# Optimization experiments

Hardware: AMD Instinct MI355X
Metric: run time of the kernel (lower is better)

Reference implementation:

```python
import jax, jax.numpy as jnp
import numpy as np

B, S, D, H = 4, 2048, 1024, 16
DH = D // H  # head dim = dim_k = dim_v


def setup_inputs() -> dict:
    key = jax.random.key(0)
    ks = jax.random.split(key, 8)
    return {
        "query": jax.random.normal(ks[0], (B, S, D), jnp.float32),
        "key": jax.random.normal(ks[1], (B, S, D), jnp.float32),
        "value": jax.random.normal(ks[2], (B, S, D), jnp.float32),
        # per-head projection weights, stacked over heads: [H, D, DH]
        "Wq": jax.random.normal(ks[3], (H, D, DH), jnp.float32) / np.sqrt(D),
        "Wk": jax.random.normal(ks[4], (H, D, DH), jnp.float32) / np.sqrt(D),
        "Wv": jax.random.normal(ks[5], (H, D, DH), jnp.float32) / np.sqrt(D),
        "Wo": jax.random.normal(ks[6], (D, D), jnp.float32) / np.sqrt(D),
        "bo": jax.random.normal(ks[7], (D,), jnp.float32) * 0.01,
        "is_causal": 1,
    }


def reference(query, key, value, Wq, Wk, Wv, Wo, bo, is_causal):
    # Per-head projections, batched over heads via einsum.  [B,H,S,DH]
    q = jnp.einsum("bsd,hdk->bhsk", query, Wq)
    k = jnp.einsum("bsd,hdk->bhsk", key, Wk)
    v = jnp.einsum("bsd,hdk->bhsk", value, Wv)
    scores = jnp.einsum("bhqk,bhsk->bhqs", q, k) / jnp.sqrt(jnp.float32(DH))
    if is_causal:
        mask = jnp.triu(jnp.ones((S, S), bool), k=1)  # strict upper tri
        scores = jnp.where(mask, -jnp.inf, scores)
    attn = jax.nn.softmax(scores, axis=-1)
    out = jnp.einsum("bhqs,bhsk->bhqk", attn, v)
    # concat heads along last dim == [B,S,H*DH], then output projection
    out = out.transpose(0, 2, 1, 3).reshape(B, S, D)
    return out @ Wo.T + bo
```

## Files before the change

kernel.cpp:

```cpp
#include <hip/hip_runtime.h>
#include <hip/hip_bf16.h>
#include <stdint.h>

typedef __bf16 bf16_t;
typedef __bf16 bf16x4 __attribute__((ext_vector_type(4)));
typedef __bf16 bf16x8 __attribute__((ext_vector_type(8)));
typedef float  f32x4  __attribute__((ext_vector_type(4)));

#define B_   4
#define S_   2048
#define D_   1024
#define H_   16
#define DH_  64
#define MTOT (B_ * S_)
#define NITEMS 1024
#define NPERS  768

__device__ __forceinline__ void gload_lds16(const void* g, void* l) {
  __builtin_amdgcn_global_load_lds((const __attribute__((address_space(1))) void*)g,
                                   (__attribute__((address_space(3))) void*)l,
                                   16, 0, 0);
}

__global__ __launch_bounds__(256) void k_cvt(const float* __restrict__ in,
                                             bf16_t* __restrict__ out, int n8) {
  for (int i = blockIdx.x * blockDim.x + threadIdx.x; i < n8;
       i += gridDim.x * blockDim.x) {
    const float4* p = (const float4*)(in + (size_t)i * 8);
    float4 a = p[0], b = p[1];
    bf16x8 o;
    o[0] = (bf16_t)a.x; o[1] = (bf16_t)a.y; o[2] = (bf16_t)a.z; o[3] = (bf16_t)a.w;
    o[4] = (bf16_t)b.x; o[5] = (bf16_t)b.y; o[6] = (bf16_t)b.z; o[7] = (bf16_t)b.w;
    *(bf16x8*)(out + (size_t)i * 8) = o;
  }
}

__global__ __launch_bounds__(256) void k_pack(const float* __restrict__ Wq,
                                              const float* __restrict__ Wk,
                                              const float* __restrict__ Wv,
                                              bf16_t* __restrict__ Wt) {
  const int z = blockIdx.z;
  const float* W = (z == 0) ? Wq : ((z == 1) ? Wk : Wv);
  const float scale = (z == 0) ? 0.125f : 1.0f;
  const int h  = blockIdx.y;
  const int d0 = blockIdx.x * 64;

  __shared__ float tile[64][65];
  const int t  = threadIdx.x;
  const int r  = t >> 2;
  const int c0 = (t & 3) * 16;

  const float* src = W + ((size_t)h * D_ + d0 + r) * DH_ + c0;
#pragma unroll
  for (int j4 = 0; j4 < 4; ++j4) {
    float4 v = *(const float4*)(src + j4 * 4);
    tile[r][c0 + j4 * 4 + 0] = v.x;
    tile[r][c0 + j4 * 4 + 1] = v.y;
    tile[r][c0 + j4 * 4 + 2] = v.z;
    tile[r][c0 + j4 * 4 + 3] = v.w;
  }
  __syncthreads();

  const int kk = r, dd0 = c0;
  bf16_t* dst = Wt + ((size_t)z * D_ + h * DH_ + kk) * D_ + d0 + dd0;
  bf16x8 o0, o1;
#pragma unroll
  for (int j = 0; j < 8; ++j) {
    o0[j] = (bf16_t)(tile[dd0 + j][kk] * scale);
    o1[j] = (bf16_t)(tile[dd0 + 8 + j][kk] * scale);
  }
  *(bf16x8*)(dst)     = o0;
  *(bf16x8*)(dst + 8) = o1;
}

template <int MODE>
__global__ __launch_bounds__(256) void k_gemm(
    const bf16_t* __restrict__ A0, const bf16_t* __restrict__ A1,
    const bf16_t* __restrict__ A2, const bf16_t* __restrict__ W,
    bf16_t* __restrict__ O0, bf16_t* __restrict__ O1, bf16_t* __restrict__ O2,
    float* __restrict__ OF, const float* __restrict__ bias,
    int M, int N, int K) {
  const int z = blockIdx.z;
  const bf16_t* A  = (MODE == 0) ? (z == 0 ? A0 : (z == 1 ? A1 : A2)) : A0;
  const bf16_t* Bt = (MODE == 0) ? (W + (size_t)z * N * K) : W;
  bf16_t* OB = (MODE == 0) ? (z == 0 ? O0 : (z == 1 ? O1 : O2)) : nullptr;

  __shared__ bf16_t As[128 * 32];
  __shared__ bf16_t Bs[128 * 32];

  const int tid  = threadIdx.x;
  const int w    = tid >> 6, lane = tid & 63;
  const int wm   = w >> 1,   wn   = w & 1;
  const int g    = lane >> 4, cl  = lane & 15;
  const int m0   = blockIdx.x * 128, n0 = blockIdx.y * 128;
  const int r_a  = lane >> 2;
  const int c_a  = (lane & 3) * 8;

  f32x4 acc[4][4] = {};

  for (int k0 = 0; k0 < K; k0 += 32) {
#pragma unroll
    for (int it = 0; it < 2; ++it) {
      const int c16 = it * 4 + w;
      const int row = c16 * 16 + r_a;
      gload_lds16(A  + (size_t)(m0 + row) * K + (k0 + c_a),
                  (bf16_t*)((char*)As + c16 * 1024));
      gload_lds16(Bt + (size_t)(n0 + row) * K + (k0 + c_a),
                  (bf16_t*)((char*)Bs + c16 * 1024));
    }
    __syncthreads();

    bf16x8 af[4], bfv[4];
#pragma unroll
    for (int mi = 0; mi < 4; ++mi)
      af[mi] = *(const bf16x8*)&As[(wm * 64 + mi * 16 + cl) * 32 + g * 8];
#pragma unroll
    for (int ni = 0; ni < 4; ++ni)
      bfv[ni] = *(const bf16x8*)&Bs[(wn * 64 + ni * 16 + cl) * 32 + g * 8];
#pragma unroll
    for (int mi = 0; mi < 4; ++mi)
#pragma unroll
      for (int ni = 0; ni < 4; ++ni)
        acc[mi][ni] = __builtin_amdgcn_mfma_f32_16x16x32_bf16(
            af[mi], bfv[ni], acc[mi][ni], 0, 0, 0);
    __syncthreads();
  }

#pragma unroll
  for (int mi = 0; mi < 4; ++mi) {
#pragma unroll
    for (int ni = 0; ni < 4; ++ni) {
      const int col = n0 + wn * 64 + ni * 16 + cl;
#pragma unroll
      for (int i = 0; i < 4; ++i) {
        const int row = m0 + wm * 64 + mi * 16 + g * 4 + i;
        if (MODE == 0)
          OB[(size_t)row * N + col] = (bf16_t)acc[mi][ni][i];
        else
          OF[(size_t)row * N + col] = acc[mi][ni][i] + bias[col];
      }
    }
  }
}

__global__ __launch_bounds__(256, 3) void k_attn(const bf16_t* __restrict__ Qp,
                                                 const bf16_t* __restrict__ Kp,
                                                 const bf16_t* __restrict__ Vp,
                                                 bf16_t* __restrict__ AO,
                                                 int* __restrict__ wq_ctr,
                                                 const int* __restrict__ causal_p) {
  __shared__ bf16_t Ks[64 * 72];
  __shared__ bf16_t Vs[2 * 64 * 64];
  __shared__ bf16_t Vt[64 * 72];
  __shared__ bf16_t Pb[4][32 * 72];
  __shared__ int s_item;

  const int tid  = threadIdx.x;
  const int w    = tid >> 6, lane = tid & 63;
  const int g    = lane >> 4, cl  = lane & 15;
  const int causal = *causal_p;
  const int gbase = (lane & 48) | ((lane & 48) >> 2);

  const int kr  = tid >> 3;
  const int kc  = (tid & 7) * 8;
  const int vd  = tid & 63;
  const int vk0 = w * 16;

  for (;;) {
    if (tid == 0) s_item = atomicAdd(wq_ctr, 1);
    __syncthreads();
    const int item = s_item;
    if (item >= NITEMS) break;

    const int qb = 15 - (item >> 6);
    const int bh = item & 63;
    const int b  = bh >> 4, h = bh & 15;
    const int q0 = qb * 128;
    const int nt = causal ? (2 * qb + 2) : (S_ >> 6);
    const int base_q = q0 + w * 32;
    const size_t base = ((size_t)b * S_) * D_ + (size_t)h * DH_;

    bf16x8 aq[2][2];
#pragma unroll
    for (int qi = 0; qi < 2; ++qi)
#pragma unroll
      for (int ks = 0; ks < 2; ++ks)
        aq[qi][ks] = *(const bf16x8*)(Qp + base + (size_t)(base_q + qi * 16 + cl) * D_ +
                                      ks * 32 + g * 8);

    f32x4 acc_o[2][4] = {};
    float m_run[2], l_run[2];
#pragma unroll
    for (int qi = 0; qi < 2; ++qi) { m_run[qi] = -1e30f; l_run[qi] = 0.f; }

    bf16x8 kreg[2];
    kreg[0] = *(const bf16x8*)(Kp + base + (size_t)(kr) * D_ + kc);
    kreg[1] = *(const bf16x8*)(Kp + base + (size_t)(32 + kr) * D_ + kc);
#pragma unroll
    for (int it = 0; it < 2; ++it) {
      const int c16 = it * 4 + w;
      gload_lds16(Vp + base + (size_t)(c16 * 8 + (lane >> 3)) * D_ + (lane & 7) * 8,
                  (char*)Vs + c16 * 1024);
    }
    *(bf16x8*)&Ks[(kr) * 72 + kc]      = kreg[0];
    *(bf16x8*)&Ks[(32 + kr) * 72 + kc] = kreg[1];
    __syncthreads();

    for (int t = 0; t < nt; ++t) {
      const int kv0 = t * 64;
      const int buf = t & 1;
      const bool pf = (t + 1 < nt);

      if (pf) {
        const int kvn = kv0 + 64;
        kreg[0] = *(const bf16x8*)(Kp + base + (size_t)(kvn + kr) * D_ + kc);
        kreg[1] = *(const bf16x8*)(Kp + base + (size_t)(kvn + 32 + kr) * D_ + kc);
#pragma unroll
        for (int it = 0; it < 2; ++it) {
          const int c16 = it * 4 + w;
          gload_lds16(Vp + base + (size_t)(kvn + c16 * 8 + (lane >> 3)) * D_ + (lane & 7) * 8,
                      (char*)Vs + (buf ^ 1) * 8192 + c16 * 1024);
        }
      }

      {
        const bf16_t* vsb = Vs + buf * 4096;
        bf16x8 w0, w1;
#pragma unroll
        for (int j = 0; j < 8; ++j) {
          w0[j] = vsb[(vk0 + j) * 64 + vd];
          w1[j] = vsb[(vk0 + 8 + j) * 64 + vd];
        }
        *(bf16x8*)&Vt[vd * 72 + vk0]     = w0;
        *(bf16x8*)&Vt[vd * 72 + vk0 + 8] = w1;
      }

      const bool active    = (!causal) || (kv0 <= base_q + 31);
      const bool need_mask = causal && (kv0 + 63 > base_q);

      if (active) {
        f32x4 sc[2][4];
#pragma unroll
        for (int qi = 0; qi < 2; ++qi)
#pragma unroll
          for (int c = 0; c < 4; ++c) sc[qi][c] = (f32x4){0.f, 0.f, 0.f, 0.f};

        __builtin_amdgcn_s_setprio(1);
#pragma unroll
        for (int c = 0; c < 4; ++c) {
          bf16x8 kf0 = *(const bf16x8*)&Ks[(c * 16 + cl) * 72 + g * 8];
          bf16x8 kf1 = *(const bf16x8*)&Ks[(c * 16 + cl) * 72 + 32 + g * 8];
#pragma unroll
          for (int qi = 0; qi < 2; ++qi) {
            sc[qi][c] = __builtin_amdgcn_mfma_f32_16x16x32_bf16(kf0, aq[qi][0], sc[qi][c], 0, 0, 0);
            sc[qi][c] = __builtin_amdgcn_mfma_f32_16x16x32_bf16(kf1, aq[qi][1], sc[qi][c], 0, 0, 0);
          }
        }
        __builtin_amdgcn_s_setprio(0);

        if (need_mask) {
#pragma unroll
          for (int qi = 0; qi < 2; ++qi) {
            const int qg = base_q + qi * 16 + cl;
#pragma unroll
            for (int c = 0; c < 4; ++c)
#pragma unroll
              for (int i = 0; i < 4; ++i) {
                const int kg = kv0 + c * 16 + g * 4 + i;
                if (kg > qg) sc[qi][c][i] = -1e30f;
              }
          }
        }

#pragma unroll
        for (int qi = 0; qi < 2; ++qi) {
          float m4[4];
#pragma unroll
          for (int c = 0; c < 4; ++c)
            m4[c] = fmaxf(fmaxf(sc[qi][c][0], sc[qi][c][1]),
                          fmaxf(sc[qi][c][2], sc[qi][c][3]));
          float m1 = fmaxf(fmaxf(m4[0], m4[1]), fmaxf(m4[2], m4[3]));
          m1 = fmaxf(m1, __shfl_xor(m1, 16));
          m1 = fmaxf(m1, __shfl_xor(m1, 32));
          if (!__all(m1 <= m_run[qi] + 8.0f)) {
            const float mnew = fmaxf(m_run[qi], m1);
            const float alpha = exp2f((m_run[qi] - mnew) * 1.44269504f);
            m_run[qi] = mnew;
            l_run[qi] *= alpha;
#pragma unroll
            for (int i = 0; i < 4; ++i) {
              const float ai = __shfl(alpha, gbase + i);
              acc_o[qi][0][i] *= ai;
              acc_o[qi][1][i] *= ai;
              acc_o[qi][2][i] *= ai;
              acc_o[qi][3][i] *= ai;
            }
          }
          float s = 0.f;
#pragma unroll
          for (int c = 0; c < 4; ++c) {
            bf16x4 pv;
#pragma unroll
            for (int i = 0; i < 4; ++i) {
              const float p = exp2f((sc[qi][c][i] - m_run[qi]) * 1.44269504f);
              s += p;
              pv[i] = (bf16_t)p;
            }
            *(bf16x4*)&Pb[w][(qi * 16 + cl) * 72 + c * 16 + ((lane >> 2) & 12)] = pv;
          }
          s += __shfl_xor(s, 16);
          s += __shfl_xor(s, 32);
          l_run[qi] += s;
        }
      }

      __syncthreads();

      if (pf) {
        *(bf16x8*)&Ks[(kr) * 72 + kc]      = kreg[0];
        *(bf16x8*)&Ks[(32 + kr) * 72 + kc] = kreg[1];
      }

      if (active) {
        __builtin_amdgcn_s_setprio(1);
#pragma unroll
        for (int ks = 0; ks < 2; ++ks) {
          bf16x8 pa0 = *(const bf16x8*)&Pb[w][(cl) * 72 + ks * 32 + g * 8];
          bf16x8 pa1 = *(const bf16x8*)&Pb[w][(16 + cl) * 72 + ks * 32 + g * 8];
#pragma unroll
          for (int dg = 0; dg < 4; ++dg) {
            bf16x8 vf = *(const bf16x8*)&Vt[(dg * 16 + cl) * 72 + ks * 32 + g * 8];
            acc_o[0][dg] = __builtin_amdgcn_mfma_f32_16x16x32_bf16(pa0, vf, acc_o[0][dg], 0, 0, 0);
            acc_o[1][dg] = __builtin_amdgcn_mfma_f32_16x16x32_bf16(pa1, vf, acc_o[1][dg], 0, 0, 0);
          }
        }
        __builtin_amdgcn_s_setprio(0);
      }

      __syncthreads();
    }

#pragma unroll
    for (int qi = 0; qi < 2; ++qi) {
      float lq[4];
#pragma unroll
      for (int i = 0; i < 4; ++i) lq[i] = __shfl(l_run[qi], gbase + i);
#pragma unroll
      for (int dg = 0; dg < 4; ++dg)
#pragma unroll
        for (int i = 0; i < 4; ++i) {
          const int q = base_q + qi * 16 + g * 4 + i;
          AO[base + (size_t)q * D_ + dg * 16 + cl] = (bf16_t)(acc_o[qi][dg][i] / lq[i]);
        }
    }
  }
}

extern "C" void kernel_launch(void* const* d_in, const int* in_sizes, int n_in,
                              void* d_out, int out_size, void* d_ws, size_t ws_size,
                              hipStream_t stream) {
  const float* query = (const float*)d_in[0];
  const float* key_  = (const float*)d_in[1];
  const float* value = (const float*)d_in[2];
  const float* Wq    = (const float*)d_in[3];
  const float* Wk    = (const float*)d_in[4];
  const float* Wv    = (const float*)d_in[5];
  const float* Wo    = (const float*)d_in[6];
  const float* bo    = (const float*)d_in[7];
  const int*   causal = (const int*)d_in[8];
  float* out = (float*)d_out;

  char* ws = (char*)d_ws;
  size_t off = 0;
  auto alloc = [&](size_t bytes) {
    char* p = ws + off;
    off += (bytes + 255) & ~(size_t)255;
    return p;
  };
  const size_t TB = (size_t)MTOT * D_ * sizeof(bf16_t);
  bf16_t* qin = (bf16_t*)alloc(TB);
  bf16_t* kin = (bf16_t*)alloc(TB);
  bf16_t* vin = (bf16_t*)alloc(TB);
  bf16_t* Qp  = (bf16_t*)alloc(TB);
  bf16_t* Kp  = (bf16_t*)alloc(TB);
  bf16_t* Vp  = (bf16_t*)alloc(TB);
  bf16_t* wt  = (bf16_t*)alloc((size_t)3 * D_ * D_ * sizeof(bf16_t));
  bf16_t* wob = (bf16_t*)alloc((size_t)D_ * D_ * sizeof(bf16_t));
  int*    ctr = (int*)alloc(256);
  bf16_t* ao  = qin;

  hipMemsetAsync(ctr, 0, sizeof(int), stream);

  const int n8 = MTOT * D_ / 8;
  k_cvt<<<2048, 256, 0, stream>>>(query, qin, n8);
  k_cvt<<<2048, 256, 0, stream>>>(key_,  kin, n8);
  k_cvt<<<2048, 256, 0, stream>>>(value, vin, n8);
  k_cvt<<<512, 256, 0, stream>>>(Wo, wob, D_ * D_ / 8);
  k_pack<<<dim3(16, 16, 3), 256, 0, stream>>>(Wq, Wk, Wv, wt);

  k_gemm<0><<<dim3(MTOT / 128, D_ / 128, 3), 256, 0, stream>>>(
      qin, kin, vin, wt, Qp, Kp, Vp, nullptr, nullptr, MTOT, D_, D_);

  k_attn<<<dim3(NPERS, 1), 256, 0, stream>>>(Qp, Kp, Vp, ao, ctr, causal);

  k_gemm<1><<<dim3(MTOT / 128, D_ / 128, 1), 256, 0, stream>>>(
      ao, nullptr, nullptr, wob, nullptr, nullptr, nullptr, out, bo, MTOT, D_, D_);
}
```

Measured before the change: 360.6 us.

## Pre-transpose V globally and double-buffer swizzled K/V tiles via direct-to-LDS loads

```diff
diff --git a/kernel.cpp b/kernel.cpp
--- a/kernel.cpp
+++ b/kernel.cpp
@@ -70,6 +70,32 @@
     o1[j] = (bf16_t)(tile[dd0 + 8 + j][kk] * scale);
   }
   *(bf16x8*)(dst)     = o0;
+  *(bf16x8*)(dst + 8) = o1;
+}
+
+__global__ __launch_bounds__(256) void k_vt(const bf16_t* __restrict__ Vp,
+                                            bf16_t* __restrict__ VpT) {
+  __shared__ bf16_t tile[64][72];
+  const int bh = blockIdx.y;
+  const int b  = bh >> 4, h = bh & 15;
+  const int s0 = blockIdx.x * 64;
+  const int t  = threadIdx.x;
+  const int r  = t >> 2;
+  const int c0 = (t & 3) * 16;
+
+  const bf16_t* src = Vp + ((size_t)(b * S_ + s0 + r)) * D_ + h * DH_ + c0;
+  *(bf16x8*)&tile[r][c0]     = *(const bf16x8*)(src);
+  *(bf16x8*)&tile[r][c0 + 8] = *(const bf16x8*)(src + 8);
+  __syncthreads();
+
+  bf16x8 o0, o1;
+#pragma unroll
+  for (int j = 0; j < 8; ++j) {
+    o0[j] = tile[c0 + j][r];
+    o1[j] = tile[c0 + 8 + j][r];
+  }
+  bf16_t* dst = VpT + ((size_t)(bh * DH_ + r)) * S_ + s0 + c0;
+  *(bf16x8*)dst       = o0;
   *(bf16x8*)(dst + 8) = o1;
 }
 
@@ -145,13 +171,12 @@
 
 __global__ __launch_bounds__(256, 3) void k_attn(const bf16_t* __restrict__ Qp,
                                                  const bf16_t* __restrict__ Kp,
-                                                 const bf16_t* __restrict__ Vp,
+                                                 const bf16_t* __restrict__ VpT,
                                                  bf16_t* __restrict__ AO,
                                                  int* __restrict__ wq_ctr,
                                                  const int* __restrict__ causal_p) {
-  __shared__ bf16_t Ks[64 * 72];
-  __shared__ bf16_t Vs[2 * 64 * 64];
-  __shared__ bf16_t Vt[64 * 72];
+  __shared__ bf16_t Ks[2 * 64 * 64];
+  __shared__ bf16_t Vt[2 * 64 * 64];
   __shared__ bf16_t Pb[4][32 * 72];
   __shared__ int s_item;
 
@@ -160,11 +185,9 @@
   const int g    = lane >> 4, cl  = lane & 15;
   const int causal = *causal_p;
   const int gbase = (lane & 48) | ((lane & 48) >> 2);
-
-  const int kr  = tid >> 3;
-  const int kc  = (tid & 7) * 8;
-  const int vd  = tid & 63;
-  const int vk0 = w * 16;
+  const int swz   = (cl & 7) << 4;
+  const int srow  = lane >> 3;
+  const int scb   = ((lane & 7) * 16) ^ (srow << 4);
 
   for (;;) {
     if (tid == 0) s_item = atomicAdd(wq_ctr, 1);
@@ -179,6 +202,7 @@
     const int nt = causal ? (2 * qb + 2) : (S_ >> 6);
     const int base_q = q0 + w * 32;
     const size_t base = ((size_t)b * S_) * D_ + (size_t)h * DH_;
+    const bf16_t* Vth = VpT + (size_t)bh * DH_ * S_;
 
     bf16x8 aq[2][2];
 #pragma unroll
@@ -193,17 +217,15 @@
 #pragma unroll
     for (int qi = 0; qi < 2; ++qi) { m_run[qi] = -1e30f; l_run[qi] = 0.f; }
 
-    bf16x8 kreg[2];
-    kreg[0] = *(const bf16x8*)(Kp + base + (size_t)(kr) * D_ + kc);
-    kreg[1] = *(const bf16x8*)(Kp + base + (size_t)(32 + kr) * D_ + kc);
 #pragma unroll
     for (int it = 0; it < 2; ++it) {
       const int c16 = it * 4 + w;
-      gload_lds16(Vp + base + (size_t)(c16 * 8 + (lane >> 3)) * D_ + (lane & 7) * 8,
-                  (char*)Vs + c16 * 1024);
+      const int row = c16 * 8 + srow;
+      gload_lds16((const char*)(Kp + base + (size_t)row * D_) + scb,
+                  (char*)Ks + c16 * 1024);
+      gload_lds16((const char*)(Vth + (size_t)row * S_) + scb,
+                  (char*)Vt + c16 * 1024);
     }
-    *(bf16x8*)&Ks[(kr) * 72 + kc]      = kreg[0];
-    *(bf16x8*)&Ks[(32 + kr) * 72 + kc] = kreg[1];
     __syncthreads();
 
     for (int t = 0; t < nt; ++t) {
@@ -213,32 +235,24 @@
 
       if (pf) {
         const int kvn = kv0 + 64;
-        kreg[0] = *(const bf16x8*)(Kp + base + (size_t)(kvn + kr) * D_ + kc);
-        kreg[1] = *(const bf16x8*)(Kp + base + (size_t)(kvn + 32 + kr) * D_ + kc);
 #pragma unroll
         for (int it = 0; it < 2; ++it) {
           const int c16 = it * 4 + w;
-          gload_lds16(Vp + base + (size_t)(kvn + c16 * 8 + (lane >> 3)) * D_ + (lane & 7) * 8,
-                      (char*)Vs + (buf ^ 1) * 8192 + c16 * 1024);
-        }
-      }
-
-      {
-        const bf16_t* vsb = Vs + buf * 4096;
-        bf16x8 w0, w1;
-#pragma unroll
-        for (int j = 0; j < 8; ++j) {
-          w0[j] = vsb[(vk0 + j) * 64 + vd];
-          w1[j] = vsb[(vk0 + 8 + j) * 64 + vd];
-        }
-        *(bf16x8*)&Vt[vd * 72 + vk0]     = w0;
-        *(bf16x8*)&Vt[vd * 72 + vk0 + 8] = w1;
+          const int row = c16 * 8 + srow;
+          gload_lds16((const char*)(Kp + base + (size_t)(kvn + row) * D_) + scb,
+                      (char*)Ks + (buf ^ 1) * 8192 + c16 * 1024);
+          gload_lds16((const char*)(Vth + (size_t)row * S_ + kvn) + scb,
+                      (char*)Vt + (buf ^ 1) * 8192 + c16 * 1024);
+        }
       }
 
       const bool active    = (!causal) || (kv0 <= base_q + 31);
       const bool need_mask = causal && (kv0 + 63 > base_q);
 
       if (active) {
+        const char* ksb = (const char*)Ks + buf * 8192;
+        const char* vtb = (const char*)Vt + buf * 8192;
+
         f32x4 sc[2][4];
 #pragma unroll
         for (int qi = 0; qi < 2; ++qi)
@@ -248,8 +262,8 @@
         __builtin_amdgcn_s_setprio(1);
 #pragma unroll
         for (int c = 0; c < 4; ++c) {
-          bf16x8 kf0 = *(const bf16x8*)&Ks[(c * 16 + cl) * 72 + g * 8];
-          bf16x8 kf1 = *(const bf16x8*)&Ks[(c * 16 + cl) * 72 + 32 + g * 8];
+          bf16x8 kf0 = *(const bf16x8*)(ksb + (c * 16 + cl) * 128 + ((g * 16) ^ swz));
+          bf16x8 kf1 = *(const bf16x8*)(ksb + (c * 16 + cl) * 128 + ((64 + g * 16) ^ swz));
 #pragma unroll
           for (int qi = 0; qi < 2; ++qi) {
             sc[qi][c] = __builtin_amdgcn_mfma_f32_16x16x32_bf16(kf0, aq[qi][0], sc[qi][c], 0, 0, 0);
@@ -312,16 +326,7 @@
           s += __shfl_xor(s, 32);
           l_run[qi] += s;
         }
-      }
-
-      __syncthreads();
-
-      if (pf) {
-        *(bf16x8*)&Ks[(kr) * 72 + kc]      = kreg[0];
-        *(bf16x8*)&Ks[(32 + kr) * 72 + kc] = kreg[1];
-      }
-
-      if (active) {
+
         __builtin_amdgcn_s_setprio(1);
 #pragma unroll
         for (int ks = 0; ks < 2; ++ks) {
@@ -329,7 +334,8 @@
           bf16x8 pa1 = *(const bf16x8*)&Pb[w][(16 + cl) * 72 + ks * 32 + g * 8];
 #pragma unroll
           for (int dg = 0; dg < 4; ++dg) {
-            bf16x8 vf = *(const bf16x8*)&Vt[(dg * 16 + cl) * 72 + ks * 32 + g * 8];
+            bf16x8 vf = *(const bf16x8*)(vtb + (dg * 16 + cl) * 128 +
+                                         ((ks * 64 + g * 16) ^ swz));
             acc_o[0][dg] = __builtin_amdgcn_mfma_f32_16x16x32_bf16(pa0, vf, acc_o[0][dg], 0, 0, 0);
             acc_o[1][dg] = __builtin_amdgcn_mfma_f32_16x16x32_bf16(pa1, vf, acc_o[1][dg], 0, 0, 0);
           }
@@ -384,6 +390,7 @@
   bf16_t* Qp  = (bf16_t*)alloc(TB);
   bf16_t* Kp  = (bf16_t*)alloc(TB);
   bf16_t* Vp  = (bf16_t*)alloc(TB);
+  bf16_t* VpT = (bf16_t*)alloc(TB);
   bf16_t* wt  = (bf16_t*)alloc((size_t)3 * D_ * D_ * sizeof(bf16_t));
   bf16_t* wob = (bf16_t*)alloc((size_t)D_ * D_ * sizeof(bf16_t));
   int*    ctr = (int*)alloc(256);
@@ -401,7 +408,9 @@
   k_gemm<0><<<dim3(MTOT / 128, D_ / 128, 3), 256, 0, stream>>>(
       qin, kin, vin, wt, Qp, Kp, Vp, nullptr, nullptr, MTOT, D_, D_);
 
-  k_attn<<<dim3(NPERS, 1), 256, 0, stream>>>(Qp, Kp, Vp, ao, ctr, causal);
+  k_vt<<<dim3(S_ / 64, B_ * H_), 256, 0, stream>>>(Vp, VpT);
+
+  k_attn<<<dim3(NPERS, 1), 256, 0, stream>>>(Qp, Kp, VpT, ao, ctr, causal);
 
   k_gemm<1><<<dim3(MTOT / 128, D_ / 128, 1), 256, 0, stream>>>(
       ao, nullptr, nullptr, wob, nullptr, nullptr, nullptr, out, bo, MTOT, D_, D_);
```

After: 371.1 us. +2.9%, slower.
